# Performance work log

Hardware: AMD Instinct MI355X
Metric: run time of the kernel (lower is better)

## Reference

```python
import jax, jax.numpy as jnp
import numpy as np

N_NODES = 100000
N_EDGES = 1000000
EDGE_F = 64
IN_C = 128
OUT_C = 256


def setup_inputs() -> dict:
    key = jax.random.key(0)
    k1, k2, k3, k4, k5, k6, k7 = jax.random.split(key, 7)
    edge_index = jax.random.randint(k1, (2, N_EDGES), 0, N_NODES, dtype=jnp.int64 if jax.config.read('jax_enable_x64') else jnp.int32)
    edge_attr = jax.random.normal(k2, (N_EDGES, EDGE_F), dtype=jnp.float32)
    node_attr = jax.random.normal(k3, (N_NODES, IN_C), dtype=jnp.float32)
    edge_weight = jax.random.uniform(k4, (N_EDGES,), dtype=jnp.float32)
    node_weight = jax.random.uniform(k5, (N_NODES,), dtype=jnp.float32)
    W = jax.random.normal(k6, (IN_C + EDGE_F, OUT_C), dtype=jnp.float32) * (1.0 / np.sqrt(IN_C + EDGE_F))
    b = jax.random.normal(k7, (OUT_C,), dtype=jnp.float32) * 0.01
    return {"edge_index": edge_index, "edge_attr": edge_attr, "node_attr": node_attr,
            "edge_weight": edge_weight, "node_weight": node_weight, "W": W, "b": b}


def reference(edge_index, edge_attr, node_attr, edge_weight, node_weight, W, b):
    num_nodes = node_attr.shape[0]
    # per-edge weighting
    ea = edge_attr * edge_weight[:, None]                       # [E, F]
    tgt = edge_index[0]                                         # [E]
    # scatter_mean over target nodes
    sums = jax.ops.segment_sum(ea, tgt, num_segments=num_nodes)                 # [N, F]
    cnt = jax.ops.segment_sum(jnp.ones_like(edge_weight), tgt, num_segments=num_nodes)  # [N]
    mean = sums / jnp.maximum(cnt, 1.0)[:, None]                # zeros for empty segments
    mean = mean * node_weight[:, None]
    x = jnp.concatenate([node_attr, mean], axis=1)              # [N, C+F]
    return jax.nn.relu(x @ W + b)                               # [N, OUT_C]
```

## Files before the change

### kernel.cpp

```cpp
#include <hip/hip_runtime.h>
#include <hip/hip_bf16.h>

#define NN 100000
#define NE 1000000
#define EF 64
#define IC 128
#define OC 256
#define CAP 48

typedef __attribute__((ext_vector_type(8))) short bf16x8;
typedef __attribute__((ext_vector_type(4))) float f32x4;

static __device__ __forceinline__ ushort f2bf(float f) {
  unsigned u = __float_as_uint(f);
  u += 0x7fffu + ((u >> 16) & 1u);
  return (ushort)(u >> 16);
}

__global__ __launch_bounds__(256) void wprep_kernel(
    const float* __restrict__ W, ushort* __restrict__ wfrag,
    int* __restrict__ cnt) {
  int t = blockIdx.x * 256 + threadIdx.x;
  int i = t & 7;
  int lane = (t >> 3) & 63;
  int ct = (t >> 9) & 15;
  int s = t >> 13;
  int k = s * 32 + (lane >> 4) * 8 + i;
  int col = ct * 16 + (lane & 15);
  wfrag[t] = f2bf(W[(size_t)k * OC + col]);
  for (int j = t; j < NN; j += 192 * 256) cnt[j] = 0;
}

__global__ __launch_bounds__(256) void place_kernel(const int4* __restrict__ tgt4,
                                                    const float4* __restrict__ ew4,
                                                    int* __restrict__ cnt,
                                                    int2* __restrict__ epack) {
  int q = blockIdx.x * 256 + threadIdx.x;
  if (q < NE / 4) {
    int4 t = tgt4[q];
    float4 w = ew4[q];
    int e = q * 4;
    int p;
    p = atomicAdd(&cnt[t.x], 1);
    if (p < CAP) epack[(size_t)t.x * CAP + p] = make_int2(e,     __float_as_int(w.x));
    p = atomicAdd(&cnt[t.y], 1);
    if (p < CAP) epack[(size_t)t.y * CAP + p] = make_int2(e + 1, __float_as_int(w.y));
    p = atomicAdd(&cnt[t.z], 1);
    if (p < CAP) epack[(size_t)t.z * CAP + p] = make_int2(e + 2, __float_as_int(w.z));
    p = atomicAdd(&cnt[t.w], 1);
    if (p < CAP) epack[(size_t)t.w * CAP + p] = make_int2(e + 3, __float_as_int(w.w));
  }
}

__global__ __launch_bounds__(256) void agg_kernel(
    const int* __restrict__ cnt, const int2* __restrict__ epack,
    const float* __restrict__ ea, const float* __restrict__ nwt,
    ushort* __restrict__ mean_bf) {
  int lane = threadIdx.x & 63;
  int wv = threadIdx.x >> 6;
  int ns = lane >> 4;
  int fq = lane & 15;
  int n = blockIdx.x * 16 + wv * 4 + ns;

  int deg = cnt[n];
  int dclamp = max(deg - 1, 0);
  const int2* strip = epack + (size_t)n * CAP;

  int md = deg;
  md = max(md, __shfl_xor(md, 16, 64));
  md = max(md, __shfl_xor(md, 32, 64));

  f32x4 acc = (f32x4)(0.0f);
  for (int j = 0; j < md; j += 8) {
#pragma unroll
    for (int u = 0; u < 8; ++u) {
      int jj = j + u;
      int c = min(jj, dclamp);
      int2 m = strip[c];
      float w = (jj < deg) ? __int_as_float(m.y) : 0.0f;
      int e = (deg > 0) ? m.x : 0;
      f32x4 v = *(const f32x4*)(ea + (size_t)e * EF + fq * 4);
      acc += v * w;
    }
  }

  float scale = nwt[n] / (float)max(deg, 1);
  ushort4 o;
  o.x = f2bf(acc[0] * scale);
  o.y = f2bf(acc[1] * scale);
  o.z = f2bf(acc[2] * scale);
  o.w = f2bf(acc[3] * scale);
  *(ushort4*)(mean_bf + (size_t)n * EF + fq * 4) = o;
}

__global__ __launch_bounds__(256) void gemm_kernel(
    const float* __restrict__ na, const ushort* __restrict__ mean_bf,
    const ushort* __restrict__ wfrag, const float* __restrict__ bias,
    float* __restrict__ out) {
  __shared__ float cs[4][16][130];
  int tid = threadIdx.x;
  int lane = tid & 63;
  int wv = tid >> 6;
  int row_base = blockIdx.x * 64 + wv * 16;
  int r = row_base + (lane & 15);
  int rc = min(r, NN - 1);
  int kofs = (lane >> 4) * 8;
  int colb = lane & 15;
  int rgrp = lane >> 4;

  const float* narow = na + (size_t)rc * IC;
  const ushort* mrow = mean_bf + (size_t)rc * EF;

  bf16x8 afrag[6];
#pragma unroll
  for (int s = 0; s < 4; ++s) {
    f32x4 lo = *(const f32x4*)(narow + s * 32 + kofs);
    f32x4 hi = *(const f32x4*)(narow + s * 32 + kofs + 4);
#pragma unroll
    for (int i = 0; i < 4; ++i) {
      afrag[s][i] = (short)f2bf(lo[i]);
      afrag[s][4 + i] = (short)f2bf(hi[i]);
    }
  }
#pragma unroll
  for (int s = 0; s < 2; ++s)
    afrag[4 + s] = *(const bf16x8*)(mrow + s * 32 + kofs);

  f32x4 acc[16];
#pragma unroll
  for (int ct = 0; ct < 16; ++ct) acc[ct] = (f32x4)(0.0f);

#pragma unroll
  for (int s = 0; s < 6; ++s) {
#pragma unroll
    for (int ct = 0; ct < 16; ++ct) {
      bf16x8 bfrag =
          *(const bf16x8*)(wfrag + ((size_t)((s * 16 + ct) * 64 + lane) * 8));
      acc[ct] =
          __builtin_amdgcn_mfma_f32_16x16x32_bf16(afrag[s], bfrag, acc[ct], 0, 0, 0);
    }
  }

#pragma unroll
  for (int h = 0; h < 2; ++h) {
#pragma unroll
    for (int t = 0; t < 8; ++t) {
      int ct = h * 8 + t;
      float bv = bias[ct * 16 + colb];
#pragma unroll
      for (int i = 0; i < 4; ++i)
        cs[wv][rgrp * 4 + i][t * 16 + colb] = fmaxf(acc[ct][i] + bv, 0.0f);
    }
    __syncthreads();
#pragma unroll
    for (int k = 0; k < 8; ++k) {
      int row = 2 * k + (lane >> 5);
      int c4 = (lane & 31) * 4;
      f32x4 v = *(const f32x4*)&cs[wv][row][c4];
      int gr = row_base + row;
      if (gr < NN)
        __builtin_nontemporal_store(v, (f32x4*)(out + (size_t)gr * OC + h * 128 + c4));
    }
    __syncthreads();
  }
}

extern "C" void kernel_launch(void* const* d_in, const int* in_sizes, int n_in,
                              void* d_out, int out_size, void* d_ws, size_t ws_size,
                              hipStream_t stream) {
  const int* edge_index = (const int*)d_in[0];
  const float* edge_attr = (const float*)d_in[1];
  const float* node_attr = (const float*)d_in[2];
  const float* edge_weight = (const float*)d_in[3];
  const float* node_weight = (const float*)d_in[4];
  const float* W = (const float*)d_in[5];
  const float* bias = (const float*)d_in[6];
  float* out = (float*)d_out;

  char* p = (char*)d_ws;
  ushort* mean_bf = (ushort*)p;
  int2* epack    = (int2*)(p + 12800000);
  int* cnt       = (int*)(p + 51200000);
  ushort* wfrag  = (ushort*)(p + 51600000);

  wprep_kernel<<<192, 256, 0, stream>>>(W, wfrag, cnt);
  place_kernel<<<(NE / 4 + 255) / 256, 256, 0, stream>>>(
      (const int4*)edge_index, (const float4*)edge_weight, cnt, epack);
  agg_kernel<<<NN / 16, 256, 0, stream>>>(cnt, epack, edge_attr,
                                          node_weight, mean_bf);
  gemm_kernel<<<(NN + 63) / 64, 256, 0, stream>>>(node_attr, mean_bf, wfrag,
                                                  bias, out);
}
```

Measured before the change: 206.2 us.

## Fuse edge aggregation into GEMM kernel via shared-memory mean tile

Merges the aggregation and GEMM kernels into one kernel. Each block first computes the scaled mean for its 64 nodes into a shared-memory bf16 tile, then runs the MFMA GEMM reading those means from LDS. This removes the global write and re-read of the mean buffer and one kernel launch. In exchange, each block does both the gather and the GEMM, so more LDS per block may lower occupancy and the gather latency is no longer overlapped across separate launches.

```diff
diff --git a/kernel.cpp b/kernel.cpp
--- a/kernel.cpp
+++ b/kernel.cpp
@@ -52,64 +52,66 @@
   }
 }
 
-__global__ __launch_bounds__(256) void agg_kernel(
+__global__ __launch_bounds__(256) void fused_kernel(
     const int* __restrict__ cnt, const int2* __restrict__ epack,
     const float* __restrict__ ea, const float* __restrict__ nwt,
-    ushort* __restrict__ mean_bf) {
-  int lane = threadIdx.x & 63;
-  int wv = threadIdx.x >> 6;
-  int ns = lane >> 4;
-  int fq = lane & 15;
-  int n = blockIdx.x * 16 + wv * 4 + ns;
+    const float* __restrict__ na, const ushort* __restrict__ wfrag,
+    const float* __restrict__ bias, float* __restrict__ out) {
+  __shared__ ushort mean_s[64][72];
+  __shared__ float cs[4][16][130];
 
-  int deg = cnt[n];
-  int dclamp = max(deg - 1, 0);
-  const int2* strip = epack + (size_t)n * CAP;
-
-  int md = deg;
-  md = max(md, __shfl_xor(md, 16, 64));
-  md = max(md, __shfl_xor(md, 32, 64));
-
-  f32x4 acc = (f32x4)(0.0f);
-  for (int j = 0; j < md; j += 8) {
-#pragma unroll
-    for (int u = 0; u < 8; ++u) {
-      int jj = j + u;
-      int c = min(jj, dclamp);
-      int2 m = strip[c];
-      float w = (jj < deg) ? __int_as_float(m.y) : 0.0f;
-      int e = (deg > 0) ? m.x : 0;
-      f32x4 v = *(const f32x4*)(ea + (size_t)e * EF + fq * 4);
-      acc += v * w;
-    }
-  }
-
-  float scale = nwt[n] / (float)max(deg, 1);
-  ushort4 o;
-  o.x = f2bf(acc[0] * scale);
-  o.y = f2bf(acc[1] * scale);
-  o.z = f2bf(acc[2] * scale);
-  o.w = f2bf(acc[3] * scale);
-  *(ushort4*)(mean_bf + (size_t)n * EF + fq * 4) = o;
-}
-
-__global__ __launch_bounds__(256) void gemm_kernel(
-    const float* __restrict__ na, const ushort* __restrict__ mean_bf,
-    const ushort* __restrict__ wfrag, const float* __restrict__ bias,
-    float* __restrict__ out) {
-  __shared__ float cs[4][16][130];
   int tid = threadIdx.x;
   int lane = tid & 63;
   int wv = tid >> 6;
-  int row_base = blockIdx.x * 64 + wv * 16;
-  int r = row_base + (lane & 15);
+  int ns = lane >> 4;
+  int fq = lane & 15;
+  int row_base = blockIdx.x * 64;
+
+  for (int k = 0; k < 4; ++k) {
+    int n_local = wv * 16 + k * 4 + ns;
+    int n = row_base + n_local;
+    int nsafe = min(n, NN - 1);
+    int deg = (n < NN) ? cnt[nsafe] : 0;
+    int dclamp = max(deg - 1, 0);
+    const int2* strip = epack + (size_t)nsafe * CAP;
+
+    int md = deg;
+    md = max(md, __shfl_xor(md, 16, 64));
+    md = max(md, __shfl_xor(md, 32, 64));
+
+    f32x4 acc = (f32x4)(0.0f);
+    for (int j = 0; j < md; j += 8) {
+#pragma unroll
+      for (int u = 0; u < 8; ++u) {
+        int jj = j + u;
+        int c = min(jj, dclamp);
+        int2 m = strip[c];
+        float w = (jj < deg) ? __int_as_float(m.y) : 0.0f;
+        int e = (deg > 0) ? m.x : 0;
+        f32x4 v = *(const f32x4*)(ea + (size_t)e * EF + fq * 4);
+        acc += v * w;
+      }
+    }
+
+    float scale = (n < NN) ? nwt[nsafe] / (float)max(deg, 1) : 0.0f;
+    ushort4 o;
+    o.x = f2bf(acc[0] * scale);
+    o.y = f2bf(acc[1] * scale);
+    o.z = f2bf(acc[2] * scale);
+    o.w = f2bf(acc[3] * scale);
+    *(ushort4*)&mean_s[n_local][fq * 4] = o;
+  }
+  __syncthreads();
+
+  int wrow = wv * 16;
+  int r = row_base + wrow + (lane & 15);
   int rc = min(r, NN - 1);
   int kofs = (lane >> 4) * 8;
   int colb = lane & 15;
   int rgrp = lane >> 4;
 
   const float* narow = na + (size_t)rc * IC;
-  const ushort* mrow = mean_bf + (size_t)rc * EF;
+  const ushort* mrow = &mean_s[wrow + (lane & 15)][0];
 
   bf16x8 afrag[6];
 #pragma unroll
@@ -157,7 +159,7 @@
       int row = 2 * k + (lane >> 5);
       int c4 = (lane & 31) * 4;
       f32x4 v = *(const f32x4*)&cs[wv][row][c4];
-      int gr = row_base + row;
+      int gr = row_base + wrow + row;
       if (gr < NN)
         __builtin_nontemporal_store(v, (f32x4*)(out + (size_t)gr * OC + h * 128 + c4));
     }
@@ -178,16 +180,13 @@
   float* out = (float*)d_out;
 
   char* p = (char*)d_ws;
-  ushort* mean_bf = (ushort*)p;
-  int2* epack    = (int2*)(p + 12800000);
-  int* cnt       = (int*)(p + 51200000);
-  ushort* wfrag  = (ushort*)(p + 51600000);
+  int2* epack    = (int2*)p;
+  int* cnt       = (int*)(p + 38400000);
+  ushort* wfrag  = (ushort*)(p + 38800000);
 
   wprep_kernel<<<192, 256, 0, stream>>>(W, wfrag, cnt);
   place_kernel<<<(NE / 4 + 255) / 256, 256, 0, stream>>>(
       (const int4*)edge_index, (const float4*)edge_weight, cnt, epack);
-  agg_kernel<<<NN / 16, 256, 0, stream>>>(cnt, epack, edge_attr,
-                                          node_weight, mean_bf);
-  gemm_kernel<<<(NN + 63) / 64, 256, 0, stream>>>(node_attr, mean_bf, wfrag,
-                                                  bias, out);
+  fused_kernel<<<(NN + 63) / 64, 256, 0, stream>>>(
+      cnt, epack, edge_attr, node_weight, node_attr, wfrag, bias, out);
 }
```

New measurement: 273.7 us. +32.7%, slower.
